# Kernel optimization log

Measured on AMD Instinct MI355X. Metric: run time of the kernel, lower is better.

The kernel has to match this reference:

```python
import jax, jax.numpy as jnp
import numpy as np

H = 32        # query heads
KV = 8        # kv heads
HD = 128      # head_dim
EPS = 1e-6
THETA = 1e6
T = 2048
D = 4096


def _rms_norm(x, w):
    # x: [T, heads, HD]
    var = jnp.mean(jnp.square(x), axis=-1, keepdims=True)
    return x * jax.lax.rsqrt(var + EPS) * w


def _rope(x, cos, sin):
    # NEOX-style rotary: split last dim in halves. x: [T, heads, HD]
    x1, x2 = jnp.split(x, 2, axis=-1)
    return jnp.concatenate([x1 * cos - x2 * sin, x2 * cos + x1 * sin], axis=-1)


def setup_inputs() -> dict:
    key = jax.random.key(0)
    k1, k2, k3 = jax.random.split(key, 3)
    s = 1.0 / np.sqrt(D)
    return {
        "positions": jnp.arange(T, dtype=jnp.int32),
        "hidden_states": jax.random.normal(k1, (T, D), dtype=jnp.float32),
        "w_qkv": jax.random.normal(k2, (D, (H + 2 * KV) * HD), dtype=jnp.float32) * s,
        "q_norm_w": jnp.ones((HD,), dtype=jnp.float32),
        "k_norm_w": jnp.ones((HD,), dtype=jnp.float32),
        "w_o": jax.random.normal(k3, (H * HD, D), dtype=jnp.float32) * s,
    }


def reference(positions, hidden_states, w_qkv, q_norm_w, k_norm_w, w_o):
    scale = HD ** -0.5
    qkv = hidden_states @ w_qkv                              # [T, (H+2KV)*HD]
    q = qkv[:, : H * HD].reshape(T, H, HD)
    k = qkv[:, H * HD : (H + KV) * HD].reshape(T, KV, HD)
    v = qkv[:, (H + KV) * HD :].reshape(T, KV, HD)

    # per-head RMSNorm on q/k (Qwen3 QK-norm)
    q = _rms_norm(q, q_norm_w)
    k = _rms_norm(k, k_norm_w)

    # RoPE
    inv_freq = 1.0 / (THETA ** (jnp.arange(0, HD, 2, dtype=jnp.float32) / HD))
    freqs = positions.astype(jnp.float32)[:, None] * inv_freq  # [T, HD/2]
    cos = jnp.cos(freqs)[:, None, :]                            # [T, 1, HD/2]
    sin = jnp.sin(freqs)[:, None, :]
    q = _rope(q, cos, sin)
    k = _rope(k, cos, sin)

    # GQA: repeat kv heads
    rep = H // KV
    k = jnp.repeat(k, rep, axis=1)                           # [T, H, HD]
    v = jnp.repeat(v, rep, axis=1)

    # causal SDPA
    scores = jnp.einsum("thd,shd->hts", q, k) * scale        # [H, T, T]
    causal = jnp.tril(jnp.ones((T, T), dtype=bool))
    scores = jnp.where(causal[None], scores, jnp.finfo(scores.dtype).min)
    probs = jax.nn.softmax(scores, axis=-1)
    attn = jnp.einsum("hts,shd->thd", probs, v).reshape(T, H * HD)

    return attn @ w_o                                        # [T, D]
```

## Files before the change

kernel.cpp:

```cpp
#include <hip/hip_runtime.h>

#define TT   2048
#define DD   4096
#define NH   32
#define NKVH 8
#define HDM  128
#define KD   4096
#define NQKV 6144

typedef unsigned short u16;
typedef short v8s __attribute__((ext_vector_type(8)));
typedef float v4f __attribute__((ext_vector_type(4)));

#define QSCALE 0.12751744547734565f
#define EOFF   17.312340490667562f

__device__ __forceinline__ u16 f2bf(float f) {
    unsigned u = __builtin_bit_cast(unsigned, f);
    u += 0x7fffu + ((u >> 16) & 1u);
    return (u16)(u >> 16);
}
__device__ __forceinline__ float bf2f(u16 h) {
    return __builtin_bit_cast(float, ((unsigned)h) << 16);
}
__device__ __forceinline__ void gl2lds16(const void* g, void* l) {
    using gv = const __attribute__((address_space(1))) void;
    using lv = __attribute__((address_space(3))) void;
    __builtin_amdgcn_global_load_lds((gv*)g, (lv*)l, 16, 0, 0);
}

__device__ __forceinline__ void transpose_tile64(const float* __restrict__ in,
                                                 u16* __restrict__ out,
                                                 int K, int N, int n0, int k0,
                                                 float* tile, int t) {
    int rc = t >> 4, cc = (t & 15) * 4;
#pragma unroll
    for (int p = 0; p < 4; ++p) {
        int k = p * 16 + rc;
        float4 v = *(const float4*)&in[(size_t)(k0 + k) * N + n0 + cc];
        tile[k * 65 + cc] = v.x; tile[k * 65 + cc + 1] = v.y;
        tile[k * 65 + cc + 2] = v.z; tile[k * 65 + cc + 3] = v.w;
    }
    __syncthreads();
    int rn = t >> 3, ck = (t & 7) * 8;
#pragma unroll
    for (int p = 0; p < 2; ++p) {
        int n = p * 32 + rn;
        v8s tv;
#pragma unroll
        for (int j = 0; j < 8; ++j) tv[j] = (short)f2bf(tile[(ck + j) * 65 + n]);
        *(v8s*)&out[(size_t)(n0 + n) * K + k0 + ck] = tv;
    }
}

__global__ __launch_bounds__(256) void prep_all_kernel(const float* __restrict__ hidden,
                                                       u16* __restrict__ hid_bf,
                                                       const int* __restrict__ positions,
                                                       float* __restrict__ cosT,
                                                       float* __restrict__ sinT,
                                                       const float* __restrict__ w_qkv,
                                                       u16* __restrict__ wqkv_t) {
    __shared__ float tile[64 * 65];
    int b = blockIdx.x;
    if (b < 4096) {
        size_t i = ((size_t)b * 256 + threadIdx.x) * 8;
        float4 a = *(const float4*)&hidden[i];
        float4 c = *(const float4*)&hidden[i + 4];
        v8s tv;
        tv[0] = (short)f2bf(a.x); tv[1] = (short)f2bf(a.y);
        tv[2] = (short)f2bf(a.z); tv[3] = (short)f2bf(a.w);
        tv[4] = (short)f2bf(c.x); tv[5] = (short)f2bf(c.y);
        tv[6] = (short)f2bf(c.z); tv[7] = (short)f2bf(c.w);
        *(v8s*)&hid_bf[i] = tv;
    } else if (b < 4608) {
        int idx = (b - 4096) * 256 + threadIdx.x;
        int tp = idx >> 6, i = idx & 63;
        float invf = exp2f(-(float)i * 0.31143075889569023f);
        float f = (float)positions[tp] * invf;
        cosT[idx] = cosf(f);
        sinT[idx] = sinf(f);
    } else {
        int bx = b - 4608;
        int n0 = (bx % 96) * 64, k0 = (bx / 96) * 64;
        transpose_tile64(w_qkv, wqkv_t, 4096, NQKV, n0, k0, tile, threadIdx.x);
    }
}

__global__ __launch_bounds__(256) void gemm_bt_kernel(
    const u16* __restrict__ A, const u16* __restrict__ Bt, float* __restrict__ C, int N)
{
    __shared__ __align__(16) u16 smem[16896];
    u16* As = smem;
    u16* Bs = smem + 8192;
    int tid = threadIdx.x;
    int wave = tid >> 6, lane = tid & 63;
    int quad = lane >> 4, l15 = lane & 15;
    int lm = l15 & 7;
    int wm = wave >> 1, wn = wave & 1;
    int m0 = blockIdx.y * 128, n0 = blockIdx.x * 128;

    v4f acc[4][4];
    v4f z4 = {0.f, 0.f, 0.f, 0.f};
#pragma unroll
    for (int mi = 0; mi < 4; ++mi)
#pragma unroll
        for (int ni = 0; ni < 4; ++ni) acc[mi][ni] = z4;

    int rsub = lane >> 3;
    int cg = (lane & 7) ^ rsub;
    const u16* Ag = &A[(size_t)m0 * KD + cg * 8];
    const u16* Bg = &Bt[(size_t)n0 * KD + cg * 8];

    for (int k0 = 0; k0 < KD; k0 += 64) {
        __syncthreads();
#pragma unroll
        for (int c = 0; c < 4; ++c) {
            int ch = wave * 4 + c;
            int row = ch * 8 + rsub;
            gl2lds16(&Ag[(size_t)row * KD + k0], &As[ch * 512]);
            gl2lds16(&Bg[(size_t)row * KD + k0], &Bs[ch * 512]);
        }
        __syncthreads();
#pragma unroll
        for (int ks = 0; ks < 2; ++ks) {
            v8s af[4], bfr[4];
#pragma unroll
            for (int mi = 0; mi < 4; ++mi) {
                int ar = wm * 64 + mi * 16 + l15;
                af[mi] = *(const v8s*)&As[ar * 64 + ((((ks << 2) + quad) ^ lm) << 3)];
            }
#pragma unroll
            for (int ni = 0; ni < 4; ++ni) {
                int br = wn * 64 + ni * 16 + l15;
                bfr[ni] = *(const v8s*)&Bs[br * 64 + ((((ks << 2) + quad) ^ lm) << 3)];
            }
#pragma unroll
            for (int mi = 0; mi < 4; ++mi)
#pragma unroll
                for (int ni = 0; ni < 4; ++ni)
                    acc[mi][ni] = __builtin_amdgcn_mfma_f32_16x16x32_bf16(
                        af[mi], bfr[ni], acc[mi][ni], 0, 0, 0);
        }
    }
#pragma unroll
    for (int mi = 0; mi < 4; ++mi)
#pragma unroll
        for (int ni = 0; ni < 4; ++ni)
#pragma unroll
            for (int r = 0; r < 4; ++r)
                C[(size_t)(m0 + wm * 64 + mi * 16 + quad * 4 + r) * N +
                  (n0 + wn * 64 + ni * 16 + l15)] = acc[mi][ni][r];
}

__global__ __launch_bounds__(512, 2) void gemm256_qkv_kernel(
    const u16* __restrict__ A, const u16* __restrict__ Bt,
    const float* __restrict__ qw, const float* __restrict__ kw,
    const float* __restrict__ cosT, const float* __restrict__ sinT,
    u16* __restrict__ Qb, u16* __restrict__ Kb, u16* __restrict__ Vt)
{
    __shared__ __align__(16) char smem_raw[131072];
    u16* lds = (u16*)smem_raw;
    const int tid = threadIdx.x;
    const int wave = tid >> 6, lane = tid & 63;
    const int quad = lane >> 4, l15 = lane & 15, lm = l15 & 7;
    const int wm = wave >> 2, wn = wave & 3;
    const int m0 = blockIdx.y * 256, n0 = blockIdx.x * 256;

    v4f acc[2][2][4][2];
    v4f z4 = {0.f, 0.f, 0.f, 0.f};
#pragma unroll
    for (int a0 = 0; a0 < 2; ++a0)
#pragma unroll
        for (int b0 = 0; b0 < 2; ++b0)
#pragma unroll
            for (int mi = 0; mi < 4; ++mi)
#pragma unroll
                for (int ni = 0; ni < 2; ++ni) acc[a0][b0][mi][ni] = z4;

    const int rsub = lane >> 3;
    const int cg = (lane & 7) ^ rsub;
    const int ch0 = wave * 2;
    const int g0 = (quad ^ lm) << 3;
    const int g1 = ((4 + quad) ^ lm) << 3;

    const u16* AgR0 = &A[((size_t)m0 + (ch0 + 0) * 8 + rsub) * KD + cg * 8];
    const u16* AgR1 = &A[((size_t)m0 + (ch0 + 1) * 8 + rsub) * KD + cg * 8];
    const u16* BgR0 = &Bt[((size_t)n0 + (ch0 + 0) * 8 + rsub) * KD + cg * 8];
    const u16* BgR1 = &Bt[((size_t)n0 + (ch0 + 1) * 8 + rsub) * KD + cg * 8];

#define STAGE_A(tt, h) do { \
    int _b = ((tt) & 1) * 32768; \
    gl2lds16(AgR0 + (size_t)(h) * 128 * KD + (size_t)(tt) * 64, \
             &lds[_b + (h) * 8192 + (ch0 + 0) * 512]); \
    gl2lds16(AgR1 + (size_t)(h) * 128 * KD + (size_t)(tt) * 64, \
             &lds[_b + (h) * 8192 + (ch0 + 1) * 512]); \
  } while (0)
#define STAGE_B(tt, h) do { \
    int _b = ((tt) & 1) * 32768 + 16384; \
    gl2lds16(BgR0 + (size_t)(h) * 128 * KD + (size_t)(tt) * 64, \
             &lds[_b + (h) * 8192 + (ch0 + 0) * 512]); \
    gl2lds16(BgR1 + (size_t)(h) * 128 * KD + (size_t)(tt) * 64, \
             &lds[_b + (h) * 8192 + (ch0 + 1) * 512]); \
  } while (0)

    v8s af[4][2], bfr[2][2];

#define PHASE(QM, QN, RDA, RDB, STAGE_CODE, WAIT_CODE) do { \
    if (RDA) { \
      _Pragma("unroll") \
      for (int mi = 0; mi < 4; ++mi) { \
        const u16* ap = &lds[bo + ((QM) * 128 + wm * 64 + mi * 16 + l15) * 64]; \
        af[mi][0] = *(const v8s*)&ap[g0]; \
        af[mi][1] = *(const v8s*)&ap[g1]; \
      } } \
    if (RDB) { \
      _Pragma("unroll") \
      for (int ni = 0; ni < 2; ++ni) { \
        const u16* bp = &lds[bo + 16384 + ((QN) * 128 + wn * 32 + ni * 16 + l15) * 64]; \
        bfr[ni][0] = *(const v8s*)&bp[g0]; \
        bfr[ni][1] = *(const v8s*)&bp[g1]; \
      } } \
    STAGE_CODE; \
    __builtin_amdgcn_s_barrier(); \
    asm volatile("s_waitcnt lgkmcnt(0)" ::: "memory"); \
    __builtin_amdgcn_s_setprio(1); \
    _Pragma("unroll") \
    for (int mi = 0; mi < 4; ++mi) \
      _Pragma("unroll") \
      for (int ni = 0; ni < 2; ++ni) { \
        acc[QM][QN][mi][ni] = __builtin_amdgcn_mfma_f32_16x16x32_bf16( \
            af[mi][0], bfr[ni][0], acc[QM][QN][mi][ni], 0, 0, 0); \
        acc[QM][QN][mi][ni] = __builtin_amdgcn_mfma_f32_16x16x32_bf16( \
            af[mi][1], bfr[ni][1], acc[QM][QN][mi][ni], 0, 0, 0); \
      } \
    __builtin_amdgcn_s_setprio(0); \
    WAIT_CODE; \
    __builtin_amdgcn_s_barrier(); \
  } while (0)

    STAGE_A(0, 0); STAGE_B(0, 0); STAGE_B(0, 1); STAGE_A(0, 1);
    STAGE_A(1, 0); STAGE_B(1, 1); STAGE_A(1, 1);
    asm volatile("s_waitcnt vmcnt(6)" ::: "memory");
    __builtin_amdgcn_s_barrier();

#pragma unroll 2
    for (int t = 0; t < 64; ++t) {
        const int bo = (t & 1) * 32768;
        PHASE(0, 0, 1, 1, { if (t + 1 < 64) STAGE_B(t + 1, 0); }, {});
        PHASE(0, 1, 0, 1, { if (t + 2 < 64) STAGE_A(t + 2, 0); }, {});
        PHASE(1, 1, 1, 0, { if (t + 2 < 64) STAGE_B(t + 2, 1); }, {});
        PHASE(1, 0, 0, 1, { if (t + 2 < 64) STAGE_A(t + 2, 1); },
              { if (t + 2 < 64) { asm volatile("s_waitcnt vmcnt(6)" ::: "memory"); }
                else            { asm volatile("s_waitcnt vmcnt(0)" ::: "memory"); } });
    }
#undef PHASE
#undef STAGE_A
#undef STAGE_B

    u16* Ct = lds;
    const int t0q = blockIdx.y * 256;
#pragma unroll
    for (int hh = 0; hh < 2; ++hh) {
        __syncthreads();
#pragma unroll
        for (int qm = 0; qm < 2; ++qm)
#pragma unroll
            for (int mi = 0; mi < 4; ++mi)
#pragma unroll
                for (int ni = 0; ni < 2; ++ni)
#pragma unroll
                    for (int r = 0; r < 4; ++r)
                        Ct[(qm * 128 + wm * 64 + mi * 16 + quad * 4 + r) * 132 +
                           wn * 32 + ni * 16 + l15] = f2bf(acc[qm][hh][mi][ni][r]);
        __syncthreads();
        const int head = blockIdx.x * 2 + hh;
        if (head < 40) {
            if (tid < 256) {
                const int row = tid;
                const float* w = (head < 32) ? qw : kw;
                float ss = 0.f;
                for (int i = 0; i < 128; ++i) {
                    float x = bf2f(Ct[row * 132 + i]);
                    ss += x * x;
                }
                float rs = rsqrtf(ss * (1.0f / 128.0f) + 1e-6f);
                if (head < 32) rs *= QSCALE;
                const int ti = t0q + row;
                for (int i = 0; i < 64; ++i) {
                    float x1 = bf2f(Ct[row * 132 + i]) * rs * w[i];
                    float x2 = bf2f(Ct[row * 132 + 64 + i]) * rs * w[64 + i];
                    float c = cosT[ti * 64 + i], s = sinT[ti * 64 + i];
                    Ct[row * 132 + i]      = f2bf(x1 * c - x2 * s);
                    Ct[row * 132 + 64 + i] = f2bf(x2 * c + x1 * s);
                }
            }
            __syncthreads();
            u16* dst = (head < 32) ? &Qb[((size_t)head * TT + t0q) * HDM]
                                   : &Kb[((size_t)(head - 32) * TT + t0q) * HDM];
            for (int cix = tid; cix < 256 * 16; cix += 512) {
                int row = cix >> 4, part = (cix & 15) * 8;
                v8s tv;
#pragma unroll
                for (int j = 0; j < 8; ++j) tv[j] = (short)Ct[row * 132 + part + j];
                *(v8s*)&dst[row * HDM + part] = tv;
            }
        } else {
            const int kvh = head - 40;
            if (tid < 128) {
                const int hd = tid;
                for (int tb = 0; tb < 32; ++tb) {
                    v8s tv;
#pragma unroll
                    for (int j = 0; j < 8; ++j) tv[j] = (short)Ct[(tb * 8 + j) * 132 + hd];
                    *(v8s*)&Vt[((size_t)kvh * HDM + hd) * TT + t0q + tb * 8] = tv;
                }
            }
        }
    }
}

__global__ __launch_bounds__(256) void attn_plus_kernel(
    const u16* __restrict__ Qb, const u16* __restrict__ Kb,
    const u16* __restrict__ Vt, u16* __restrict__ Ob,
    const float* __restrict__ w_o, u16* __restrict__ wo_t)
{
    __shared__ __align__(16) char smem_raw[40960];
    int tid = threadIdx.x;
    if (blockIdx.x >= 1024) {
        int bx = blockIdx.x - 1024;
        int n0 = (bx & 63) * 64, k0 = (bx >> 6) * 64;
        transpose_tile64(w_o, wo_t, 4096, 4096, n0, k0, (float*)smem_raw, tid);
        return;
    }
    u16* Kl = (u16*)smem_raw;
    u16* Vl = (u16*)(smem_raw + 16384);
    u16* Pl = (u16*)(smem_raw + 32768);
    int wave = tid >> 6, lane = tid & 63;
    int quad = lane >> 4, l15 = lane & 15;
    int idx = blockIdx.x;
    int h = idx & 31;
    int qb = 31 - (idx >> 5);
    int kv = h >> 2;
    int q0 = qb * 64;
    int lm = l15 & 7;

    v8s qf[4];
    {
        const u16* qr = &Qb[((size_t)h * TT + q0 + wave * 16 + l15) * HDM];
#pragma unroll
        for (int ks = 0; ks < 4; ++ks) qf[ks] = *(const v8s*)&qr[ks * 32 + quad * 8];
    }

    v4f z4 = {0.f, 0.f, 0.f, 0.f};
    v4f of[8];
#pragma unroll
    for (int i = 0; i < 8; ++i) of[i] = z4;
    float lsum[4];
#pragma unroll
    for (int r = 0; r < 4; ++r) lsum[r] = 0.f;
    u16* Pw = &Pl[wave * 1024];

    for (int s0 = 0; s0 <= q0; s0 += 64) {
        __syncthreads();
#pragma unroll
        for (int c = 0; c < 4; ++c) {
            int ch = wave * 4 + c;
            int rk = ch * 4 + (lane >> 4);
            int ck = (lane & 15) ^ (rk & 7);
            gl2lds16(&Kb[((size_t)kv * TT + s0 + rk) * HDM + ck * 8], &Kl[ch * 512]);
            int rv = ch * 8 + (lane >> 3);
            int cv = (lane & 7) ^ (rv & 7);
            gl2lds16(&Vt[((size_t)kv * HDM + rv) * TT + s0 + cv * 8], &Vl[ch * 512]);
        }
        __syncthreads();
        v4f sf[4];
#pragma unroll
        for (int nt = 0; nt < 4; ++nt) {
            v4f cacc = z4;
#pragma unroll
            for (int ks = 0; ks < 4; ++ks)
                cacc = __builtin_amdgcn_mfma_f32_16x16x32_bf16(
                    qf[ks],
                    *(const v8s*)&Kl[(nt * 16 + l15) * 128 + (((ks * 4 + quad) ^ lm) << 3)],
                    cacc, 0, 0, 0);
            sf[nt] = cacc;
        }
        if (s0 == q0) {
#pragma unroll
            for (int nt = 0; nt < 4; ++nt) {
                int sg = s0 + nt * 16 + l15;
#pragma unroll
                for (int r = 0; r < 4; ++r) {
                    int qg = q0 + wave * 16 + quad * 4 + r;
                    if (sg > qg) sf[nt][r] = -3.0e38f;
                }
            }
        }
#pragma unroll
        for (int nt = 0; nt < 4; ++nt)
#pragma unroll
            for (int r = 0; r < 4; ++r) {
                float p = exp2f(sf[nt][r] - EOFF);
                sf[nt][r] = p;
                lsum[r] += p;
            }
#pragma unroll
        for (int nt = 0; nt < 4; ++nt)
#pragma unroll
            for (int r = 0; r < 4; ++r) {
                int row = quad * 4 + r;
                int pch = ((nt << 1) + (l15 >> 3)) ^ (row & 7);
                Pw[row * 64 + pch * 8 + (l15 & 7)] = f2bf(sf[nt][r]);
            }
#pragma unroll
        for (int sub = 0; sub < 2; ++sub) {
            v8s pa = *(const v8s*)&Pw[l15 * 64 + ((((sub << 2) + quad) ^ lm) << 3)];
#pragma unroll
            for (int nt = 0; nt < 8; ++nt)
                of[nt] = __builtin_amdgcn_mfma_f32_16x16x32_bf16(
                    pa,
                    *(const v8s*)&Vl[(nt * 16 + l15) * 64 + ((((sub << 2) + quad) ^ lm) << 3)],
                    of[nt], 0, 0, 0);
        }
    }
#pragma unroll
    for (int off = 1; off < 16; off <<= 1)
#pragma unroll
        for (int r = 0; r < 4; ++r) lsum[r] += __shfl_xor(lsum[r], off, 64);
    float invl[4];
#pragma unroll
    for (int r = 0; r < 4; ++r) invl[r] = 1.0f / lsum[r];
#pragma unroll
    for (int nt = 0; nt < 8; ++nt)
#pragma unroll
        for (int r = 0; r < 4; ++r)
            Ob[(size_t)(q0 + wave * 16 + quad * 4 + r) * (NH * HDM) + h * HDM + nt * 16 + l15] =
                f2bf(of[nt][r] * invl[r]);
}

extern "C" void kernel_launch(void* const* d_in, const int* in_sizes, int n_in,
                              void* d_out, int out_size, void* d_ws, size_t ws_size,
                              hipStream_t stream)
{
    (void)in_sizes; (void)n_in; (void)out_size; (void)ws_size;
    const int*   positions = (const int*)d_in[0];
    const float* hidden    = (const float*)d_in[1];
    const float* w_qkv     = (const float*)d_in[2];
    const float* q_norm_w  = (const float*)d_in[3];
    const float* k_norm_w  = (const float*)d_in[4];
    const float* w_o       = (const float*)d_in[5];
    float* out = (float*)d_out;
    char* ws = (char*)d_ws;
    char* ob = (char*)d_out;

    u16* hid_bf = (u16*)(ws + 0);
    u16* attnO  = (u16*)(ws + 0);
    u16* wqkv_t = (u16*)(ws + (size_t)16777216);
    u16* wo_t   = (u16*)(ws + (size_t)16777216);

    u16*   Qb   = (u16*)(ob + 0);
    u16*   Kb   = (u16*)(ob + (size_t)16777216);
    u16*   Vt   = (u16*)(ob + (size_t)20971520);
    float* cosT = (float*)(ob + (size_t)25165824);
    float* sinT = (float*)(ob + (size_t)25690112);

    prep_all_kernel<<<10752, 256, 0, stream>>>(hidden, hid_bf, positions, cosT, sinT,
                                               w_qkv, wqkv_t);

    gemm256_qkv_kernel<<<dim3(24, 8), 512, 0, stream>>>(
        hid_bf, wqkv_t, q_norm_w, k_norm_w, cosT, sinT, Qb, Kb, Vt);

    attn_plus_kernel<<<5120, 256, 0, stream>>>(Qb, Kb, Vt, attnO, w_o, wo_t);

    gemm_bt_kernel<<<dim3(32, 16), 256, 0, stream>>>(attnO, wo_t, out, 4096);
}
```

Before: 481.6 us.

## Retile QKV GEMM to 128x384 blocks with 256-block grid and parallel epilogue

```diff
diff --git a/kernel.cpp b/kernel.cpp
--- a/kernel.cpp
+++ b/kernel.cpp
@@ -152,7 +152,7 @@
                   (n0 + wn * 64 + ni * 16 + l15)] = acc[mi][ni][r];
 }
 
-__global__ __launch_bounds__(512, 2) void gemm256_qkv_kernel(
+__global__ __launch_bounds__(512, 2) void gemm_qkv384_kernel(
     const u16* __restrict__ A, const u16* __restrict__ Bt,
     const float* __restrict__ qw, const float* __restrict__ kw,
     const float* __restrict__ cosT, const float* __restrict__ sinT,
@@ -164,18 +164,16 @@
     const int wave = tid >> 6, lane = tid & 63;
     const int quad = lane >> 4, l15 = lane & 15, lm = l15 & 7;
     const int wm = wave >> 2, wn = wave & 3;
-    const int m0 = blockIdx.y * 256, n0 = blockIdx.x * 256;
-
-    v4f acc[2][2][4][2];
+    const int m0 = blockIdx.y * 128, n0 = blockIdx.x * 384;
+
+    v4f acc[2][4][3];
     v4f z4 = {0.f, 0.f, 0.f, 0.f};
 #pragma unroll
-    for (int a0 = 0; a0 < 2; ++a0)
-#pragma unroll
-        for (int b0 = 0; b0 < 2; ++b0)
-#pragma unroll
-            for (int mi = 0; mi < 4; ++mi)
-#pragma unroll
-                for (int ni = 0; ni < 2; ++ni) acc[a0][b0][mi][ni] = z4;
+    for (int nh = 0; nh < 2; ++nh)
+#pragma unroll
+        for (int mi = 0; mi < 4; ++mi)
+#pragma unroll
+            for (int ni = 0; ni < 3; ++ni) acc[nh][mi][ni] = z4;
 
     const int rsub = lane >> 3;
     const int cg = (lane & 7) ^ rsub;
@@ -188,38 +186,31 @@
     const u16* BgR0 = &Bt[((size_t)n0 + (ch0 + 0) * 8 + rsub) * KD + cg * 8];
     const u16* BgR1 = &Bt[((size_t)n0 + (ch0 + 1) * 8 + rsub) * KD + cg * 8];
 
-#define STAGE_A(tt, h) do { \
+#define STAGE_AH(tt) do { \
     int _b = ((tt) & 1) * 32768; \
-    gl2lds16(AgR0 + (size_t)(h) * 128 * KD + (size_t)(tt) * 64, \
-             &lds[_b + (h) * 8192 + (ch0 + 0) * 512]); \
-    gl2lds16(AgR1 + (size_t)(h) * 128 * KD + (size_t)(tt) * 64, \
-             &lds[_b + (h) * 8192 + (ch0 + 1) * 512]); \
+    gl2lds16(AgR0 + (size_t)(tt) * 64, &lds[_b + (ch0 + 0) * 512]); \
+    gl2lds16(AgR1 + (size_t)(tt) * 64, &lds[_b + (ch0 + 1) * 512]); \
   } while (0)
-#define STAGE_B(tt, h) do { \
-    int _b = ((tt) & 1) * 32768 + 16384; \
+#define STAGE_BH(tt, h) do { \
+    int _b = ((tt) & 1) * 32768 + 8192; \
     gl2lds16(BgR0 + (size_t)(h) * 128 * KD + (size_t)(tt) * 64, \
              &lds[_b + (h) * 8192 + (ch0 + 0) * 512]); \
     gl2lds16(BgR1 + (size_t)(h) * 128 * KD + (size_t)(tt) * 64, \
              &lds[_b + (h) * 8192 + (ch0 + 1) * 512]); \
   } while (0)
 
-    v8s af[4][2], bfr[2][2];
-
-#define PHASE(QM, QN, RDA, RDB, STAGE_CODE, WAIT_CODE) do { \
+    v8s af[4], bfr[3];
+
+#define PHASEX(BO, G, NHI, RDA, STAGE_CODE, WAIT_CODE) do { \
     if (RDA) { \
       _Pragma("unroll") \
-      for (int mi = 0; mi < 4; ++mi) { \
-        const u16* ap = &lds[bo + ((QM) * 128 + wm * 64 + mi * 16 + l15) * 64]; \
-        af[mi][0] = *(const v8s*)&ap[g0]; \
-        af[mi][1] = *(const v8s*)&ap[g1]; \
-      } } \
-    if (RDB) { \
-      _Pragma("unroll") \
-      for (int ni = 0; ni < 2; ++ni) { \
-        const u16* bp = &lds[bo + 16384 + ((QN) * 128 + wn * 32 + ni * 16 + l15) * 64]; \
-        bfr[ni][0] = *(const v8s*)&bp[g0]; \
-        bfr[ni][1] = *(const v8s*)&bp[g1]; \
-      } } \
+      for (int mi = 0; mi < 4; ++mi) \
+        af[mi] = *(const v8s*)&lds[(BO) + (wm * 64 + mi * 16 + l15) * 64 + (G)]; \
+    } \
+    _Pragma("unroll") \
+    for (int ni = 0; ni < 3; ++ni) \
+      bfr[ni] = *(const v8s*)&lds[(BO) + 8192 + \
+                   (wn * 96 + (NHI) * 48 + ni * 16 + l15) * 64 + (G)]; \
     STAGE_CODE; \
     __builtin_amdgcn_s_barrier(); \
     asm volatile("s_waitcnt lgkmcnt(0)" ::: "memory"); \
@@ -227,93 +218,101 @@
     _Pragma("unroll") \
     for (int mi = 0; mi < 4; ++mi) \
       _Pragma("unroll") \
-      for (int ni = 0; ni < 2; ++ni) { \
-        acc[QM][QN][mi][ni] = __builtin_amdgcn_mfma_f32_16x16x32_bf16( \
-            af[mi][0], bfr[ni][0], acc[QM][QN][mi][ni], 0, 0, 0); \
-        acc[QM][QN][mi][ni] = __builtin_amdgcn_mfma_f32_16x16x32_bf16( \
-            af[mi][1], bfr[ni][1], acc[QM][QN][mi][ni], 0, 0, 0); \
-      } \
+      for (int ni = 0; ni < 3; ++ni) \
+        acc[NHI][mi][ni] = __builtin_amdgcn_mfma_f32_16x16x32_bf16( \
+            af[mi], bfr[ni], acc[NHI][mi][ni], 0, 0, 0); \
     __builtin_amdgcn_s_setprio(0); \
     WAIT_CODE; \
     __builtin_amdgcn_s_barrier(); \
   } while (0)
 
-    STAGE_A(0, 0); STAGE_B(0, 0); STAGE_B(0, 1); STAGE_A(0, 1);
-    STAGE_A(1, 0); STAGE_B(1, 1); STAGE_A(1, 1);
-    asm volatile("s_waitcnt vmcnt(6)" ::: "memory");
+#define VM0 asm volatile("s_waitcnt vmcnt(0)" ::: "memory")
+
+#define TILE_MAIN(BO, TT1) do { \
+    PHASEX(BO, g0, 0, 1, { STAGE_AH(TT1); STAGE_BH(TT1, 0); }, {}); \
+    PHASEX(BO, g0, 1, 0, { STAGE_BH(TT1, 1); }, {}); \
+    PHASEX(BO, g1, 0, 1, { STAGE_BH(TT1, 2); }, {}); \
+    PHASEX(BO, g1, 1, 0, {}, { VM0; }); \
+  } while (0)
+
+    STAGE_AH(0); STAGE_BH(0, 0); STAGE_BH(0, 1); STAGE_BH(0, 2);
+    VM0;
     __builtin_amdgcn_s_barrier();
 
 #pragma unroll 2
-    for (int t = 0; t < 64; ++t) {
+    for (int t = 0; t < 62; ++t) {
         const int bo = (t & 1) * 32768;
-        PHASE(0, 0, 1, 1, { if (t + 1 < 64) STAGE_B(t + 1, 0); }, {});
-        PHASE(0, 1, 0, 1, { if (t + 2 < 64) STAGE_A(t + 2, 0); }, {});
-        PHASE(1, 1, 1, 0, { if (t + 2 < 64) STAGE_B(t + 2, 1); }, {});
-        PHASE(1, 0, 0, 1, { if (t + 2 < 64) STAGE_A(t + 2, 1); },
-              { if (t + 2 < 64) { asm volatile("s_waitcnt vmcnt(6)" ::: "memory"); }
-                else            { asm volatile("s_waitcnt vmcnt(0)" ::: "memory"); } });
-    }
-#undef PHASE
-#undef STAGE_A
-#undef STAGE_B
+        TILE_MAIN(bo, t + 1);
+    }
+    TILE_MAIN(0, 63);
+    PHASEX(32768, g0, 0, 1, {}, {});
+    PHASEX(32768, g0, 1, 0, {}, {});
+    PHASEX(32768, g1, 0, 1, {}, {});
+    PHASEX(32768, g1, 1, 0, {}, {});
+#undef TILE_MAIN
+#undef PHASEX
+#undef STAGE_AH
+#undef STAGE_BH
+#undef VM0
 
     u16* Ct = lds;
-    const int t0q = blockIdx.y * 256;
-#pragma unroll
-    for (int hh = 0; hh < 2; ++hh) {
-        __syncthreads();
-#pragma unroll
-        for (int qm = 0; qm < 2; ++qm)
-#pragma unroll
-            for (int mi = 0; mi < 4; ++mi)
-#pragma unroll
-                for (int ni = 0; ni < 2; ++ni)
-#pragma unroll
-                    for (int r = 0; r < 4; ++r)
-                        Ct[(qm * 128 + wm * 64 + mi * 16 + quad * 4 + r) * 132 +
-                           wn * 32 + ni * 16 + l15] = f2bf(acc[qm][hh][mi][ni][r]);
-        __syncthreads();
-        const int head = blockIdx.x * 2 + hh;
+    const int t0q = blockIdx.y * 128;
+    __syncthreads();
+#pragma unroll
+    for (int nh = 0; nh < 2; ++nh)
+#pragma unroll
+        for (int mi = 0; mi < 4; ++mi)
+#pragma unroll
+            for (int ni = 0; ni < 3; ++ni)
+#pragma unroll
+                for (int r = 0; r < 4; ++r)
+                    Ct[(wm * 64 + mi * 16 + quad * 4 + r) * 392 +
+                       wn * 96 + nh * 48 + ni * 16 + l15] = f2bf(acc[nh][mi][ni][r]);
+    __syncthreads();
+    if (tid < 384) {
+        const int row = tid & 127, hh = tid >> 7;
+        const int head = blockIdx.x * 3 + hh;
         if (head < 40) {
-            if (tid < 256) {
-                const int row = tid;
-                const float* w = (head < 32) ? qw : kw;
-                float ss = 0.f;
-                for (int i = 0; i < 128; ++i) {
-                    float x = bf2f(Ct[row * 132 + i]);
-                    ss += x * x;
-                }
-                float rs = rsqrtf(ss * (1.0f / 128.0f) + 1e-6f);
-                if (head < 32) rs *= QSCALE;
-                const int ti = t0q + row;
-                for (int i = 0; i < 64; ++i) {
-                    float x1 = bf2f(Ct[row * 132 + i]) * rs * w[i];
-                    float x2 = bf2f(Ct[row * 132 + 64 + i]) * rs * w[64 + i];
-                    float c = cosT[ti * 64 + i], s = sinT[ti * 64 + i];
-                    Ct[row * 132 + i]      = f2bf(x1 * c - x2 * s);
-                    Ct[row * 132 + 64 + i] = f2bf(x2 * c + x1 * s);
-                }
-            }
-            __syncthreads();
+            const float* w = (head < 32) ? qw : kw;
+            float ss = 0.f;
+            for (int i = 0; i < 128; ++i) {
+                float x = bf2f(Ct[row * 392 + hh * 128 + i]);
+                ss += x * x;
+            }
+            float rs = rsqrtf(ss * (1.0f / 128.0f) + 1e-6f);
+            if (head < 32) rs *= QSCALE;
+            const int ti = t0q + row;
+            for (int i = 0; i < 64; ++i) {
+                float x1 = bf2f(Ct[row * 392 + hh * 128 + i]) * rs * w[i];
+                float x2 = bf2f(Ct[row * 392 + hh * 128 + 64 + i]) * rs * w[64 + i];
+                float c = cosT[ti * 64 + i], s = sinT[ti * 64 + i];
+                Ct[row * 392 + hh * 128 + i]      = f2bf(x1 * c - x2 * s);
+                Ct[row * 392 + hh * 128 + 64 + i] = f2bf(x2 * c + x1 * s);
+            }
+        }
+    }
+    __syncthreads();
+#pragma unroll
+    for (int hh = 0; hh < 3; ++hh) {
+        const int head = blockIdx.x * 3 + hh;
+        if (head < 40) {
             u16* dst = (head < 32) ? &Qb[((size_t)head * TT + t0q) * HDM]
                                    : &Kb[((size_t)(head - 32) * TT + t0q) * HDM];
-            for (int cix = tid; cix < 256 * 16; cix += 512) {
+            for (int cix = tid; cix < 128 * 16; cix += 512) {
                 int row = cix >> 4, part = (cix & 15) * 8;
                 v8s tv;
 #pragma unroll
-                for (int j = 0; j < 8; ++j) tv[j] = (short)Ct[row * 132 + part + j];
+                for (int j = 0; j < 8; ++j) tv[j] = (short)Ct[row * 392 + hh * 128 + part + j];
                 *(v8s*)&dst[row * HDM + part] = tv;
             }
         } else {
             const int kvh = head - 40;
-            if (tid < 128) {
-                const int hd = tid;
-                for (int tb = 0; tb < 32; ++tb) {
-                    v8s tv;
-#pragma unroll
-                    for (int j = 0; j < 8; ++j) tv[j] = (short)Ct[(tb * 8 + j) * 132 + hd];
-                    *(v8s*)&Vt[((size_t)kvh * HDM + hd) * TT + t0q + tb * 8] = tv;
-                }
+            for (int cix = tid; cix < 128 * 16; cix += 512) {
+                int hd = cix >> 4, tb = cix & 15;
+                v8s tv;
+#pragma unroll
+                for (int j = 0; j < 8; ++j) tv[j] = (short)Ct[(tb * 8 + j) * 392 + hh * 128 + hd];
+                *(v8s*)&Vt[((size_t)kvh * HDM + hd) * TT + t0q + tb * 8] = tv;
             }
         }
     }
@@ -467,7 +466,7 @@
     prep_all_kernel<<<10752, 256, 0, stream>>>(hidden, hid_bf, positions, cosT, sinT,
                                                w_qkv, wqkv_t);
 
-    gemm256_qkv_kernel<<<dim3(24, 8), 512, 0, stream>>>(
+    gemm_qkv384_kernel<<<dim3(16, 16), 512, 0, stream>>>(
         hid_bf, wqkv_t, q_norm_w, k_norm_w, cosT, sinT, Qb, Kb, Vt);
 
     attn_plus_kernel<<<5120, 256, 0, stream>>>(Qb, Kb, Vt, attnO, w_o, wo_t);
```

Measured after the change: 456.9 us. 1.05x faster.
